# Kernel tuning notes

Measured on AMD Instinct MI355X. Metric: run time of the kernel, lower is better.

The kernel has to match this reference:

```python
import jax, jax.numpy as jnp
import numpy as np

B, T, S, C, E, H = 4, 2048, 2048, 256, 512, 8
D = E // H
SCALE = E ** (-0.5)


def setup_inputs() -> dict:
    key = jax.random.key(0)
    ks = jax.random.split(key, 12)
    x = jax.random.normal(ks[0], (B, T, C), dtype=jnp.float32)
    context = jax.random.normal(ks[1], (B, S, E), dtype=jnp.float32)
    pad_mask = jax.random.randint(ks[2], (B, T, S), 0, 2) == 1
    p = 0.02
    # Conv1d kernel_size=1 weights stored squeezed: [out_ch, in_ch]
    w_in = jax.random.normal(ks[3], (E, C), dtype=jnp.float32) * p
    b_in = jnp.zeros((E,), dtype=jnp.float32)
    wq = jax.random.normal(ks[4], (E, E), dtype=jnp.float32) * p
    bq = jnp.zeros((E,), dtype=jnp.float32)
    wk = jax.random.normal(ks[5], (E, E), dtype=jnp.float32) * p
    bk = jnp.zeros((E,), dtype=jnp.float32)
    wv = jax.random.normal(ks[6], (E, E), dtype=jnp.float32) * p
    bv = jnp.zeros((E,), dtype=jnp.float32)
    w_out = jax.random.normal(ks[7], (C, E), dtype=jnp.float32) * p
    b_out = jnp.zeros((C,), dtype=jnp.float32)
    return {"x": x, "context": context, "pad_mask": pad_mask,
            "w_in": w_in, "b_in": b_in, "wq": wq, "bq": bq,
            "wk": wk, "bk": bk, "wv": wv, "bv": bv,
            "w_out": w_out, "b_out": b_out}


def reference(x, context, pad_mask, w_in, b_in, wq, bq, wk, bk, wv, bv, w_out, b_out):
    # proj_in: Conv1d k=1 == per-token linear on channel dim. [B,T,C] -> [B,T,E]
    xe = jnp.einsum('btc,ec->bte', x, w_in) + b_in
    Q = (xe @ wq.T + bq).reshape(B, T, H, D)       # query tokens
    K = (context @ wk.T + bk).reshape(B, S, H, D)  # key tokens
    V = (context @ wv.T + bv).reshape(B, S, H, D)
    att = jnp.einsum('bihd,bjhd->bhij', Q, K) * SCALE  # [B,H,T,S]
    att = jnp.where(pad_mask[:, None, :, :], jnp.float32(-1e9), att)
    att = jax.nn.softmax(att, axis=-1)
    out = jnp.einsum('bhij,bjhd->bihd', att, V).reshape(B, T, E)
    # proj_out: Conv1d k=1, [B,T,E] -> [B,T,C]
    out = jnp.einsum('bte,ce->btc', out, w_out) + b_out
    return out
```

## Files before the change

### kernel.cpp

```cpp
#include <hip/hip_runtime.h>
#include <cstdint>
#include <cstddef>

#define Bb 4
#define Tt 2048
#define Ssz 2048
#define Cc 256
#define Ee 512
#define Hh 8
#define LDK 1024

typedef short bf8 __attribute__((ext_vector_type(8)));
typedef float f4 __attribute__((ext_vector_type(4)));

__device__ __forceinline__ unsigned short f2bf(float x) {
  unsigned int u = __float_as_uint(x);
  u += 0x7fffu + ((u >> 16) & 1u);
  return (unsigned short)(u >> 16);
}

template <bool OUT_BF16, int BM, int BN, int WGM>
__device__ __forceinline__ void gemm_core(unsigned short (*As)[72],
                                          unsigned short (*Bs)[72],
                                          const unsigned short* __restrict__ A,
                                          const unsigned short* __restrict__ Bt,
                                          const float* __restrict__ bias0,
                                          const float* __restrict__ bias1, int split,
                                          void* __restrict__ Cout,
                                          int M, int N, int K, int m0, int n0) {
  constexpr int WGN = 4 / WGM;
  constexpr int MI = BM / (WGM * 16);
  constexpr int NJ = BN / (WGN * 16);
  constexpr int NA = BM / 32;
  constexpr int NB = BN / 32;
  const int tid = threadIdx.x;
  const int wave = tid >> 6, lane = tid & 63;
  const int lrow = lane & 15, quad = lane >> 4;
  const int wm = (wave / WGN) * (BM / WGM);
  const int wn = (wave % WGN) * (BN / WGN);
  const int arow = tid >> 3, ac = tid & 7;

  f4 acc[MI][NJ];
#pragma unroll
  for (int i = 0; i < MI; i++)
#pragma unroll
    for (int j = 0; j < NJ; j++) {
      f4 z = {0.f, 0.f, 0.f, 0.f};
      acc[i][j] = z;
    }

  bf8 apre[NA], bpre[NB];
#pragma unroll
  for (int i = 0; i < NA; i++)
    apre[i] = *(const bf8*)(A + (size_t)(m0 + arow + i * 32) * K + ac * 8);
#pragma unroll
  for (int i = 0; i < NB; i++)
    bpre[i] = *(const bf8*)(Bt + (size_t)(n0 + arow + i * 32) * K + ac * 8);

  const int nkt = K >> 6;
  for (int kt = 0; kt < nkt; ++kt) {
#pragma unroll
    for (int i = 0; i < NA; i++) *(bf8*)&As[arow + i * 32][ac * 8] = apre[i];
#pragma unroll
    for (int i = 0; i < NB; i++) *(bf8*)&Bs[arow + i * 32][ac * 8] = bpre[i];
    __syncthreads();
    if (kt + 1 < nkt) {
      int k0 = (kt + 1) << 6;
#pragma unroll
      for (int i = 0; i < NA; i++)
        apre[i] = *(const bf8*)(A + (size_t)(m0 + arow + i * 32) * K + k0 + ac * 8);
#pragma unroll
      for (int i = 0; i < NB; i++)
        bpre[i] = *(const bf8*)(Bt + (size_t)(n0 + arow + i * 32) * K + k0 + ac * 8);
    }
#pragma unroll
    for (int kk = 0; kk < 2; kk++) {
      bf8 af[MI], bff[NJ];
#pragma unroll
      for (int i = 0; i < MI; i++)
        af[i] = *(const bf8*)&As[wm + i * 16 + lrow][kk * 32 + quad * 8];
#pragma unroll
      for (int j = 0; j < NJ; j++)
        bff[j] = *(const bf8*)&Bs[wn + j * 16 + lrow][kk * 32 + quad * 8];
#pragma unroll
      for (int i = 0; i < MI; i++)
#pragma unroll
        for (int j = 0; j < NJ; j++)
          acc[i][j] = __builtin_amdgcn_mfma_f32_16x16x32_bf16(af[i], bff[j],
                                                              acc[i][j], 0, 0, 0);
    }
    __syncthreads();
  }

#pragma unroll
  for (int j = 0; j < NJ; j++) {
    int col = n0 + wn + j * 16 + lrow;
    float bvv = 0.f;
    if (bias0) bvv = (col < split) ? bias0[col] : bias1[col - split];
#pragma unroll
    for (int i = 0; i < MI; i++) {
#pragma unroll
      for (int r = 0; r < 4; r++) {
        int row = m0 + wm + i * 16 + quad * 4 + r;
        float v = acc[i][j][r] + bvv;
        if (OUT_BF16)
          ((unsigned short*)Cout)[(size_t)row * N + col] = f2bf(v);
        else
          ((float*)Cout)[(size_t)row * N + col] = v;
      }
    }
  }
}

template <bool OUT_BF16, int BM, int BN, int WGM>
__global__ __launch_bounds__(256) void gemm_bt(const unsigned short* __restrict__ A,
                                               const unsigned short* __restrict__ Bt,
                                               const float* __restrict__ bias0,
                                               const float* __restrict__ bias1, int split,
                                               void* __restrict__ Cout,
                                               int M, int N, int K) {
  __shared__ unsigned short As[BM][72];
  __shared__ unsigned short Bs[BN][72];
  gemm_core<OUT_BF16, BM, BN, WGM>(As, Bs, A, Bt, bias0, bias1, split, Cout, M, N, K,
                                   blockIdx.x * BM, blockIdx.y * BN);
}

__global__ __launch_bounds__(256) void prep(const float* __restrict__ x,
                                            const float* __restrict__ ctx,
                                            const float* __restrict__ w_in,
                                            const float* __restrict__ b_in,
                                            const float* __restrict__ wq,
                                            const float* __restrict__ bq,
                                            const float* __restrict__ wk,
                                            const float* __restrict__ wv,
                                            const float* __restrict__ wo,
                                            unsigned short* __restrict__ xb,
                                            unsigned short* __restrict__ cb,
                                            unsigned short* __restrict__ wkvb,
                                            unsigned short* __restrict__ wob,
                                            unsigned short* __restrict__ wqin,
                                            float* __restrict__ bqinb, float qsc) {
  __shared__ unsigned short sh[128][72];
  const int bid = blockIdx.x, tid = threadIdx.x;
  if (bid < 6144) {
    const float* s;
    unsigned short* d;
    int i;
    if (bid < 2048) { s = x; d = xb; i = bid * 256 + tid; }
    else            { s = ctx; d = cb; i = (bid - 2048) * 256 + tid; }
    float4 v = ((const float4*)s)[i];
    ushort4 o;
    o.x = f2bf(v.x); o.y = f2bf(v.y); o.z = f2bf(v.z); o.w = f2bf(v.w);
    ((ushort4*)d)[i] = o;
  } else if (bid < 6784) {
    int i = (bid - 6144) * 256 + tid;
    const float* s;
    unsigned short* d;
    int off;
    if (i < 131072)      { s = wk; d = wkvb; off = i; }
    else                 { s = wo; d = wob; off = i - 131072; }
    if (i >= 65536 && i < 131072) { s = wv; off = i - 65536; d = wkvb + 262144; }
    float4 v = ((const float4*)s)[off];
    ushort4 o;
    o.x = f2bf(v.x); o.y = f2bf(v.y); o.z = f2bf(v.z); o.w = f2bf(v.w);
    ((ushort4*)d)[off] = o;
  } else if (bid < 6816) {
    const int idx = bid - 6784;
    const int m0 = (idx & 7) * 64, n0 = (idx >> 3) * 64;
    unsigned short (*As)[72] = (unsigned short (*)[72]) & sh[0][0];
    unsigned short (*Bs)[72] = (unsigned short (*)[72]) & sh[64][0];
    const int wave = tid >> 6, lane = tid & 63;
    const int lrow = lane & 15, quad = lane >> 4;
    const int wm = (wave >> 1) * 32, wn = (wave & 1) * 32;
    const int arow = tid >> 3, ac = tid & 7;
    f4 acc[2][2];
#pragma unroll
    for (int i = 0; i < 2; i++)
#pragma unroll
      for (int j = 0; j < 2; j++) {
        f4 z = {0.f, 0.f, 0.f, 0.f};
        acc[i][j] = z;
      }
    for (int kt = 0; kt < 8; kt++) {
#pragma unroll
      for (int i = 0; i < 2; i++) {
        int row = arow + i * 32;
        const float* src = wq + (size_t)(m0 + row) * Ee + kt * 64 + ac * 8;
        float4 v0 = *(const float4*)src, v1 = *(const float4*)(src + 4);
        bf8 av;
        av[0] = (short)f2bf(v0.x * qsc); av[1] = (short)f2bf(v0.y * qsc);
        av[2] = (short)f2bf(v0.z * qsc); av[3] = (short)f2bf(v0.w * qsc);
        av[4] = (short)f2bf(v1.x * qsc); av[5] = (short)f2bf(v1.y * qsc);
        av[6] = (short)f2bf(v1.z * qsc); av[7] = (short)f2bf(v1.w * qsc);
        *(bf8*)&As[row][ac * 8] = av;
        int c = n0 + row;
        bf8 bv;
#pragma unroll
        for (int k = 0; k < 8; k++)
          bv[k] = (short)f2bf(w_in[(size_t)(kt * 64 + ac * 8 + k) * Cc + c]);
        *(bf8*)&Bs[row][ac * 8] = bv;
      }
      __syncthreads();
#pragma unroll
      for (int kk = 0; kk < 2; kk++) {
        bf8 af[2], bff[2];
#pragma unroll
        for (int i = 0; i < 2; i++) af[i] = *(const bf8*)&As[wm + i * 16 + lrow][kk * 32 + quad * 8];
#pragma unroll
        for (int j = 0; j < 2; j++) bff[j] = *(const bf8*)&Bs[wn + j * 16 + lrow][kk * 32 + quad * 8];
#pragma unroll
        for (int i = 0; i < 2; i++)
#pragma unroll
          for (int j = 0; j < 2; j++)
            acc[i][j] = __builtin_amdgcn_mfma_f32_16x16x32_bf16(af[i], bff[j], acc[i][j], 0, 0, 0);
      }
      __syncthreads();
    }
#pragma unroll
    for (int j = 0; j < 2; j++)
#pragma unroll
      for (int i = 0; i < 2; i++)
#pragma unroll
        for (int r = 0; r < 4; r++)
          wqin[(size_t)(m0 + wm + i * 16 + quad * 4 + r) * Cc + n0 + wn + j * 16 + lrow] =
              f2bf(acc[i][j][r]);
  } else {
    const int o = (bid - 6816) * 32 + (tid >> 3);
    const int k0 = (tid & 7) * 64;
    float s = 0.f;
#pragma unroll
    for (int i = 0; i < 16; i++) {
      float4 w = *(const float4*)(wq + (size_t)o * Ee + k0 + i * 4);
      float4 bb = *(const float4*)(b_in + k0 + i * 4);
      s += w.x * bb.x + w.y * bb.y + w.z * bb.z + w.w * bb.w;
    }
    s += __shfl_xor(s, 1);
    s += __shfl_xor(s, 2);
    s += __shfl_xor(s, 4);
    if ((tid & 7) == 0) bqinb[o] = (s + bq[o]) * qsc;
  }
}

__global__ __launch_bounds__(256) void kvpack(const unsigned short* __restrict__ cb,
                                              const unsigned short* __restrict__ wkv,
                                              const float* __restrict__ bk,
                                              const float* __restrict__ bv,
                                              unsigned short* __restrict__ KVout,
                                              const int* __restrict__ mask,
                                              unsigned int* __restrict__ mp) {
  __shared__ unsigned short As[128][72];
  __shared__ unsigned short Bs[128][72];
  const int bid = blockIdx.x;
  if (bid < 512) {
    gemm_core<true, 128, 128, 2>(As, Bs, cb, wkv, bk, bv, 512, KVout, 8192, 1024, 512,
                                 (bid & 63) * 128, (bid >> 6) * 128);
  } else {
    int i = (bid - 512) * 256 + threadIdx.x;
    const int4* src = (const int4*)mask + (size_t)i * 8;
    unsigned int w = 0;
#pragma unroll
    for (int k = 0; k < 8; k++) {
      int4 v = src[k];
      w |= (unsigned int)(v.x != 0) << (k * 4);
      w |= (unsigned int)(v.y != 0) << (k * 4 + 1);
      w |= (unsigned int)(v.z != 0) << (k * 4 + 2);
      w |= (unsigned int)(v.w != 0) << (k * 4 + 3);
    }
    mp[i] = w;
  }
}

__global__ __launch_bounds__(256) void vtrans(const unsigned short* __restrict__ V, int ldv,
                                              unsigned short* __restrict__ Vt) {
  __shared__ unsigned short tile[64][72];
  const int tid = threadIdx.x;
  const int b = blockIdx.z, h = blockIdx.y, s0 = blockIdx.x * 64;
#pragma unroll
  for (int i = 0; i < 2; i++) {
    int id = tid + i * 256;
    int row = id >> 3, c = id & 7;
    *(bf8*)&tile[row][c * 8] =
        *(const bf8*)(V + (size_t)(b * Ssz + s0 + row) * ldv + h * 64 + c * 8);
  }
  __syncthreads();
#pragma unroll
  for (int i = 0; i < 2; i++) {
    int id = tid + i * 256;
    int d = id >> 3, c = id & 7;
    bf8 o;
#pragma unroll
    for (int k = 0; k < 8; k++) {
      int kk = (k + d) & 7;
      o[kk] = (short)tile[c * 8 + kk][d];
    }
    *(bf8*)(Vt + (size_t)((b * Hh + h) * 64 + d) * Ssz + s0 + c * 8) = o;
  }
}

__global__ __launch_bounds__(256) void attn(const unsigned short* __restrict__ Q,
                                            const unsigned short* __restrict__ K,
                                            const unsigned short* __restrict__ Vt,
                                            const unsigned int* __restrict__ mp,
                                            unsigned short* __restrict__ O) {
  __shared__ unsigned short Ks[2][64][72];
  __shared__ unsigned short Vts[2][64][72];
  __shared__ unsigned short Ps[128][72];
  const int tid = threadIdx.x;
  const int wave = tid >> 6, lane = tid & 63;
  const int lrow = lane & 15, quad = lane >> 4;
  const int b = blockIdx.z, h = blockIdx.y, t0 = blockIdx.x * 128;
  const int arow = tid >> 3, ac = tid & 7;
  const int wm = wave * 32;

#pragma unroll
  for (int i = 0; i < 4; i++) {
    int row = arow + i * 32;
    *(bf8*)&Ps[row][ac * 8] =
        *(const bf8*)(Q + (size_t)(b * Tt + t0 + row) * Ee + h * 64 + ac * 8);
  }
  __syncthreads();
  bf8 qf[2][2];
#pragma unroll
  for (int mi = 0; mi < 2; mi++) {
    qf[mi][0] = *(const bf8*)&Ps[wm + mi * 16 + lrow][quad * 8];
    qf[mi][1] = *(const bf8*)&Ps[wm + mi * 16 + lrow][32 + quad * 8];
  }

  f4 oacc[2][4];
  f4 dacc[2];
#pragma unroll
  for (int mi = 0; mi < 2; mi++) {
    f4 z = {0.f, 0.f, 0.f, 0.f};
    dacc[mi] = z;
#pragma unroll
    for (int j = 0; j < 4; j++) oacc[mi][j] = z;
  }
  bf8 ones;
#pragma unroll
  for (int k = 0; k < 8; k++) ones[k] = (short)0x3F80;

  const unsigned short* Kbase = K + (size_t)b * Ssz * LDK + h * 64;
  const unsigned short* Vbase = Vt + (size_t)((b * Hh + h) * 64) * Ssz;
  const unsigned int* mrow0 = mp + (size_t)(b * Tt + t0 + wm + lrow) * 64;
  const unsigned int* mrow1 = mp + (size_t)(b * Tt + t0 + wm + 16 + lrow) * 64;

  bf8 kreg[2], vreg[2];
#pragma unroll
  for (int i = 0; i < 2; i++) {
    int row = arow + i * 32;
    kreg[i] = *(const bf8*)(Kbase + (size_t)row * LDK + ac * 8);
    vreg[i] = *(const bf8*)(Vbase + (size_t)row * Ssz + ac * 8);
  }

  int buf = 0;
  for (int s0 = 0; s0 < Ssz; s0 += 64) {
#pragma unroll
    for (int i = 0; i < 2; i++) {
      int row = arow + i * 32;
      *(bf8*)&Ks[buf][row][ac * 8] = kreg[i];
      *(bf8*)&Vts[buf][row][ac * 8] = vreg[i];
    }
    __syncthreads();
    if (s0 + 64 < Ssz) {
#pragma unroll
      for (int i = 0; i < 2; i++) {
        int row = arow + i * 32;
        kreg[i] = *(const bf8*)(Kbase + (size_t)(s0 + 64 + row) * LDK + ac * 8);
        vreg[i] = *(const bf8*)(Vbase + (size_t)row * Ssz + s0 + 64 + ac * 8);
      }
    }
    const uint2 mw0 = *(const uint2*)(mrow0 + (s0 >> 5));
    const uint2 mw1 = *(const uint2*)(mrow1 + (s0 >> 5));

#pragma unroll
    for (int sf = 0; sf < 4; sf++) {
      bf8 kf0 = *(const bf8*)&Ks[buf][sf * 16 + lrow][quad * 8];
      bf8 kf1 = *(const bf8*)&Ks[buf][sf * 16 + lrow][32 + quad * 8];
      f4 sa[2];
      f4 z = {0.f, 0.f, 0.f, 0.f};
      sa[0] = z; sa[1] = z;
      sa[0] = __builtin_amdgcn_mfma_f32_16x16x32_bf16(kf0, qf[0][0], sa[0], 0, 0, 0);
      sa[0] = __builtin_amdgcn_mfma_f32_16x16x32_bf16(kf1, qf[0][1], sa[0], 0, 0, 0);
      sa[1] = __builtin_amdgcn_mfma_f32_16x16x32_bf16(kf0, qf[1][0], sa[1], 0, 0, 0);
      sa[1] = __builtin_amdgcn_mfma_f32_16x16x32_bf16(kf1, qf[1][1], sa[1], 0, 0, 0);
#pragma unroll
      for (int mi = 0; mi < 2; mi++) {
        const uint2 mw = mi ? mw1 : mw0;
        const unsigned int w = (sf >= 2) ? mw.y : mw.x;
        ushort4 pk;
#pragma unroll
        for (int r = 0; r < 4; r++) {
          const unsigned int bit = (sf & 1) * 16 + quad * 4 + r;
          float e = __builtin_amdgcn_exp2f(sa[mi][r]);
          float p = ((w >> bit) & 1u) ? 0.f : e;
          unsigned short pb = (unsigned short)(__float_as_uint(p) >> 16);
          if (r == 0) pk.x = pb;
          else if (r == 1) pk.y = pb;
          else if (r == 2) pk.z = pb;
          else pk.w = pb;
        }
        *(ushort4*)&Ps[wm + mi * 16 + lrow][sf * 16 + quad * 4] = pk;
      }
    }
#pragma unroll
    for (int kk = 0; kk < 2; kk++) {
      bf8 pf[2];
#pragma unroll
      for (int mi = 0; mi < 2; mi++) {
        pf[mi] = *(const bf8*)&Ps[wm + mi * 16 + lrow][kk * 32 + quad * 8];
        dacc[mi] = __builtin_amdgcn_mfma_f32_16x16x32_bf16(pf[mi], ones, dacc[mi], 0, 0, 0);
      }
#pragma unroll
      for (int j = 0; j < 4; j++) {
        bf8 vf = *(const bf8*)&Vts[buf][j * 16 + lrow][kk * 32 + quad * 8];
#pragma unroll
        for (int mi = 0; mi < 2; mi++)
          oacc[mi][j] = __builtin_amdgcn_mfma_f32_16x16x32_bf16(pf[mi], vf, oacc[mi][j], 0, 0, 0);
      }
    }
    buf ^= 1;
  }

#pragma unroll
  for (int mi = 0; mi < 2; mi++) {
#pragma unroll
    for (int r = 0; r < 4; r++) {
      float inv = 1.0f / dacc[mi][r];
      int row = b * Tt + t0 + wm + mi * 16 + quad * 4 + r;
#pragma unroll
      for (int j = 0; j < 4; j++)
        O[(size_t)row * Ee + h * 64 + j * 16 + lrow] = f2bf(oacc[mi][j][r] * inv);
    }
  }
}

extern "C" void kernel_launch(void* const* d_in, const int* in_sizes, int n_in,
                              void* d_out, int out_size, void* d_ws, size_t ws_size,
                              hipStream_t stream) {
  const float* x    = (const float*)d_in[0];
  const float* ctx  = (const float*)d_in[1];
  const int*   mask = (const int*)d_in[2];
  const float* w_in = (const float*)d_in[3];
  const float* b_in = (const float*)d_in[4];
  const float* wq   = (const float*)d_in[5];
  const float* bq   = (const float*)d_in[6];
  const float* wk   = (const float*)d_in[7];
  const float* bk   = (const float*)d_in[8];
  const float* wv   = (const float*)d_in[9];
  const float* bv   = (const float*)d_in[10];
  const float* wo   = (const float*)d_in[11];
  const float* bo   = (const float*)d_in[12];

  const float qsc = 0.04419417382415922f * 1.4426950408889634f;

  unsigned short* ws = (unsigned short*)d_ws;
  unsigned short* xb    = ws;
  unsigned short* cb    = ws + 2097152;
  unsigned short* wkvb  = ws + 6291456;
  unsigned short* wob   = ws + 6815744;
  unsigned short* wqin  = ws + 6946816;
  float*          bqinb = (float*)(ws + 7077888);
  unsigned short* Qb    = ws + 7208960;
  unsigned short* KVb   = ws + 11403264;
  unsigned short* Ob    = ws + 19791872;
  unsigned int*   maskp = (unsigned int*)xb;
  unsigned short* Vtb   = cb;

  prep<<<6832, 256, 0, stream>>>(x, ctx, w_in, b_in, wq, bq, wk, wv, wo,
                                 xb, cb, wkvb, wob, wqin, bqinb, qsc);
  gemm_bt<true, 128, 64, 2><<<dim3(64, 8), 256, 0, stream>>>(
      xb, wqin, bqinb, nullptr, 512, Qb, 8192, 512, 256);
  kvpack<<<2560, 256, 0, stream>>>(cb, wkvb, bk, bv, KVb, mask, maskp);
  vtrans<<<dim3(32, 8, 4), 256, 0, stream>>>(KVb + 512, LDK, Vtb);
  attn<<<dim3(16, 8, 4), 256, 0, stream>>>(Qb, KVb, Vtb, maskp, Ob);
  gemm_bt<false, 64, 64, 2><<<dim3(128, 4), 256, 0, stream>>>(
      Ob, wob, bo, nullptr, 256, d_out, 8192, 256, 512);
}
```

Measured before the change: 252.6 us.

## Fuse Q/K/V projections into one kernel with inline fp32 conversion and V-transpose epilogue

Removes the separate fp32-to-bf16 conversion pass for x and context by converting inside the GEMM A-tile load. Merges the Q and K/V projection GEMMs into one launch, and writes V directly in transposed layout so the vtrans kernel is dropped. Mask packing moves into prep. The attention kernel now handles 256 query rows per block (64 per wave), doubling register accumulators. This halves the grid, which may lower occupancy.

```diff
diff --git a/kernel.cpp b/kernel.cpp
--- a/kernel.cpp
+++ b/kernel.cpp
@@ -8,7 +8,6 @@
 #define Cc 256
 #define Ee 512
 #define Hh 8
-#define LDK 1024
 
 typedef short bf8 __attribute__((ext_vector_type(8)));
 typedef float f4 __attribute__((ext_vector_type(4)));
@@ -19,114 +18,16 @@
   return (unsigned short)(u >> 16);
 }
 
-template <bool OUT_BF16, int BM, int BN, int WGM>
-__device__ __forceinline__ void gemm_core(unsigned short (*As)[72],
-                                          unsigned short (*Bs)[72],
-                                          const unsigned short* __restrict__ A,
-                                          const unsigned short* __restrict__ Bt,
-                                          const float* __restrict__ bias0,
-                                          const float* __restrict__ bias1, int split,
-                                          void* __restrict__ Cout,
-                                          int M, int N, int K, int m0, int n0) {
-  constexpr int WGN = 4 / WGM;
-  constexpr int MI = BM / (WGM * 16);
-  constexpr int NJ = BN / (WGN * 16);
-  constexpr int NA = BM / 32;
-  constexpr int NB = BN / 32;
-  const int tid = threadIdx.x;
-  const int wave = tid >> 6, lane = tid & 63;
-  const int lrow = lane & 15, quad = lane >> 4;
-  const int wm = (wave / WGN) * (BM / WGM);
-  const int wn = (wave % WGN) * (BN / WGN);
-  const int arow = tid >> 3, ac = tid & 7;
-
-  f4 acc[MI][NJ];
-#pragma unroll
-  for (int i = 0; i < MI; i++)
-#pragma unroll
-    for (int j = 0; j < NJ; j++) {
-      f4 z = {0.f, 0.f, 0.f, 0.f};
-      acc[i][j] = z;
-    }
-
-  bf8 apre[NA], bpre[NB];
-#pragma unroll
-  for (int i = 0; i < NA; i++)
-    apre[i] = *(const bf8*)(A + (size_t)(m0 + arow + i * 32) * K + ac * 8);
-#pragma unroll
-  for (int i = 0; i < NB; i++)
-    bpre[i] = *(const bf8*)(Bt + (size_t)(n0 + arow + i * 32) * K + ac * 8);
-
-  const int nkt = K >> 6;
-  for (int kt = 0; kt < nkt; ++kt) {
-#pragma unroll
-    for (int i = 0; i < NA; i++) *(bf8*)&As[arow + i * 32][ac * 8] = apre[i];
-#pragma unroll
-    for (int i = 0; i < NB; i++) *(bf8*)&Bs[arow + i * 32][ac * 8] = bpre[i];
-    __syncthreads();
-    if (kt + 1 < nkt) {
-      int k0 = (kt + 1) << 6;
-#pragma unroll
-      for (int i = 0; i < NA; i++)
-        apre[i] = *(const bf8*)(A + (size_t)(m0 + arow + i * 32) * K + k0 + ac * 8);
-#pragma unroll
-      for (int i = 0; i < NB; i++)
-        bpre[i] = *(const bf8*)(Bt + (size_t)(n0 + arow + i * 32) * K + k0 + ac * 8);
-    }
-#pragma unroll
-    for (int kk = 0; kk < 2; kk++) {
-      bf8 af[MI], bff[NJ];
-#pragma unroll
-      for (int i = 0; i < MI; i++)
-        af[i] = *(const bf8*)&As[wm + i * 16 + lrow][kk * 32 + quad * 8];
-#pragma unroll
-      for (int j = 0; j < NJ; j++)
-        bff[j] = *(const bf8*)&Bs[wn + j * 16 + lrow][kk * 32 + quad * 8];
-#pragma unroll
-      for (int i = 0; i < MI; i++)
-#pragma unroll
-        for (int j = 0; j < NJ; j++)
-          acc[i][j] = __builtin_amdgcn_mfma_f32_16x16x32_bf16(af[i], bff[j],
-                                                              acc[i][j], 0, 0, 0);
-    }
-    __syncthreads();
-  }
-
-#pragma unroll
-  for (int j = 0; j < NJ; j++) {
-    int col = n0 + wn + j * 16 + lrow;
-    float bvv = 0.f;
-    if (bias0) bvv = (col < split) ? bias0[col] : bias1[col - split];
-#pragma unroll
-    for (int i = 0; i < MI; i++) {
-#pragma unroll
-      for (int r = 0; r < 4; r++) {
-        int row = m0 + wm + i * 16 + quad * 4 + r;
-        float v = acc[i][j][r] + bvv;
-        if (OUT_BF16)
-          ((unsigned short*)Cout)[(size_t)row * N + col] = f2bf(v);
-        else
-          ((float*)Cout)[(size_t)row * N + col] = v;
-      }
-    }
-  }
-}
-
-template <bool OUT_BF16, int BM, int BN, int WGM>
-__global__ __launch_bounds__(256) void gemm_bt(const unsigned short* __restrict__ A,
-                                               const unsigned short* __restrict__ Bt,
-                                               const float* __restrict__ bias0,
-                                               const float* __restrict__ bias1, int split,
-                                               void* __restrict__ Cout,
-                                               int M, int N, int K) {
-  __shared__ unsigned short As[BM][72];
-  __shared__ unsigned short Bs[BN][72];
-  gemm_core<OUT_BF16, BM, BN, WGM>(As, Bs, A, Bt, bias0, bias1, split, Cout, M, N, K,
-                                   blockIdx.x * BM, blockIdx.y * BN);
-}
-
-__global__ __launch_bounds__(256) void prep(const float* __restrict__ x,
-                                            const float* __restrict__ ctx,
+__device__ __forceinline__ bf8 cvt8(float4 a, float4 b) {
+  bf8 r;
+  r[0] = (short)f2bf(a.x); r[1] = (short)f2bf(a.y);
+  r[2] = (short)f2bf(a.z); r[3] = (short)f2bf(a.w);
+  r[4] = (short)f2bf(b.x); r[5] = (short)f2bf(b.y);
+  r[6] = (short)f2bf(b.z); r[7] = (short)f2bf(b.w);
+  return r;
+}
+
+__global__ __launch_bounds__(256) void prep(const int* __restrict__ mask,
                                             const float* __restrict__ w_in,
                                             const float* __restrict__ b_in,
                                             const float* __restrict__ wq,
@@ -134,38 +35,42 @@
                                             const float* __restrict__ wk,
                                             const float* __restrict__ wv,
                                             const float* __restrict__ wo,
-                                            unsigned short* __restrict__ xb,
-                                            unsigned short* __restrict__ cb,
+                                            unsigned int* __restrict__ mp,
                                             unsigned short* __restrict__ wkvb,
                                             unsigned short* __restrict__ wob,
                                             unsigned short* __restrict__ wqin,
                                             float* __restrict__ bqinb, float qsc) {
   __shared__ unsigned short sh[128][72];
   const int bid = blockIdx.x, tid = threadIdx.x;
-  if (bid < 6144) {
-    const float* s;
-    unsigned short* d;
-    int i;
-    if (bid < 2048) { s = x; d = xb; i = bid * 256 + tid; }
-    else            { s = ctx; d = cb; i = (bid - 2048) * 256 + tid; }
-    float4 v = ((const float4*)s)[i];
-    ushort4 o;
-    o.x = f2bf(v.x); o.y = f2bf(v.y); o.z = f2bf(v.z); o.w = f2bf(v.w);
-    ((ushort4*)d)[i] = o;
-  } else if (bid < 6784) {
-    int i = (bid - 6144) * 256 + tid;
-    const float* s;
-    unsigned short* d;
-    int off;
-    if (i < 131072)      { s = wk; d = wkvb; off = i; }
-    else                 { s = wo; d = wob; off = i - 131072; }
-    if (i >= 65536 && i < 131072) { s = wv; off = i - 65536; d = wkvb + 262144; }
+  if (bid < 2048) {
+    int i = bid * 256 + tid;
+    const int4* src = (const int4*)mask + (size_t)i * 8;
+    unsigned int w = 0;
+#pragma unroll
+    for (int k = 0; k < 8; k++) {
+      int4 v = src[k];
+      w |= (unsigned int)(v.x != 0) << (k * 4);
+      w |= (unsigned int)(v.y != 0) << (k * 4 + 1);
+      w |= (unsigned int)(v.z != 0) << (k * 4 + 2);
+      w |= (unsigned int)(v.w != 0) << (k * 4 + 3);
+    }
+    mp[i] = w;
+  } else if (bid < 2560) {
+    int i = (bid - 2048) * 256 + tid;
+    const float* s = (i < 65536) ? wk : wv;
+    int off = (i < 65536) ? i : i - 65536;
     float4 v = ((const float4*)s)[off];
     ushort4 o;
     o.x = f2bf(v.x); o.y = f2bf(v.y); o.z = f2bf(v.z); o.w = f2bf(v.w);
-    ((ushort4*)d)[off] = o;
-  } else if (bid < 6816) {
-    const int idx = bid - 6784;
+    ((ushort4*)wkvb)[i] = o;
+  } else if (bid < 2688) {
+    int i = (bid - 2560) * 256 + tid;
+    float4 v = ((const float4*)wo)[i];
+    ushort4 o;
+    o.x = f2bf(v.x); o.y = f2bf(v.y); o.z = f2bf(v.z); o.w = f2bf(v.w);
+    ((ushort4*)wob)[i] = o;
+  } else if (bid < 2720) {
+    const int idx = bid - 2688;
     const int m0 = (idx & 7) * 64, n0 = (idx >> 3) * 64;
     unsigned short (*As)[72] = (unsigned short (*)[72]) & sh[0][0];
     unsigned short (*Bs)[72] = (unsigned short (*)[72]) & sh[64][0];
@@ -225,7 +130,7 @@
           wqin[(size_t)(m0 + wm + i * 16 + quad * 4 + r) * Cc + n0 + wn + j * 16 + lrow] =
               f2bf(acc[i][j][r]);
   } else {
-    const int o = (bid - 6816) * 32 + (tid >> 3);
+    const int o = (bid - 2720) * 32 + (tid >> 3);
     const int k0 = (tid & 7) * 64;
     float s = 0.f;
 #pragma unroll
@@ -241,59 +146,222 @@
   }
 }
 
-__global__ __launch_bounds__(256) void kvpack(const unsigned short* __restrict__ cb,
-                                              const unsigned short* __restrict__ wkv,
-                                              const float* __restrict__ bk,
-                                              const float* __restrict__ bv,
-                                              unsigned short* __restrict__ KVout,
-                                              const int* __restrict__ mask,
-                                              unsigned int* __restrict__ mp) {
+__global__ __launch_bounds__(256) void qkv(const float* __restrict__ x,
+                                           const float* __restrict__ ctx,
+                                           const unsigned short* __restrict__ wqin,
+                                           const float* __restrict__ bqinb,
+                                           const unsigned short* __restrict__ wkv,
+                                           const float* __restrict__ bk,
+                                           const float* __restrict__ bv,
+                                           unsigned short* __restrict__ Qb,
+                                           unsigned short* __restrict__ Kb,
+                                           unsigned short* __restrict__ Vt) {
   __shared__ unsigned short As[128][72];
   __shared__ unsigned short Bs[128][72];
-  const int bid = blockIdx.x;
-  if (bid < 512) {
-    gemm_core<true, 128, 128, 2>(As, Bs, cb, wkv, bk, bv, 512, KVout, 8192, 1024, 512,
-                                 (bid & 63) * 128, (bid >> 6) * 128);
+  const int bid = blockIdx.x, tid = threadIdx.x;
+  const bool isQ = bid < 256;
+  const int idx = isQ ? bid : bid - 256;
+  const int m0 = (idx & 63) * 128;
+  const int n0 = (idx >> 6) * 128;
+  const int K = isQ ? 256 : 512;
+  const float* A = isQ ? x : ctx;
+  const unsigned short* Bt = isQ ? wqin : wkv;
+
+  const int wave = tid >> 6, lane = tid & 63;
+  const int lrow = lane & 15, quad = lane >> 4;
+  const int wm = (wave >> 1) * 64, wn = (wave & 1) * 64;
+  const int arow = tid >> 3, ac = tid & 7;
+
+  f4 acc[4][4];
+#pragma unroll
+  for (int i = 0; i < 4; i++)
+#pragma unroll
+    for (int j = 0; j < 4; j++) {
+      f4 z = {0.f, 0.f, 0.f, 0.f};
+      acc[i][j] = z;
+    }
+
+  float4 ap0[4], ap1[4];
+  bf8 bpre[4];
+#pragma unroll
+  for (int i = 0; i < 4; i++) {
+    const float* src = A + (size_t)(m0 + arow + i * 32) * K + ac * 8;
+    ap0[i] = *(const float4*)src;
+    ap1[i] = *(const float4*)(src + 4);
+    bpre[i] = *(const bf8*)(Bt + (size_t)(n0 + arow + i * 32) * K + ac * 8);
+  }
+
+  const int nkt = K >> 6;
+  for (int kt = 0; kt < nkt; ++kt) {
+#pragma unroll
+    for (int i = 0; i < 4; i++) {
+      *(bf8*)&As[arow + i * 32][ac * 8] = cvt8(ap0[i], ap1[i]);
+      *(bf8*)&Bs[arow + i * 32][ac * 8] = bpre[i];
+    }
+    __syncthreads();
+    if (kt + 1 < nkt) {
+      int k0 = (kt + 1) << 6;
+#pragma unroll
+      for (int i = 0; i < 4; i++) {
+        const float* src = A + (size_t)(m0 + arow + i * 32) * K + k0 + ac * 8;
+        ap0[i] = *(const float4*)src;
+        ap1[i] = *(const float4*)(src + 4);
+        bpre[i] = *(const bf8*)(Bt + (size_t)(n0 + arow + i * 32) * K + k0 + ac * 8);
+      }
+    }
+#pragma unroll
+    for (int kk = 0; kk < 2; kk++) {
+      bf8 af[4], bff[4];
+#pragma unroll
+      for (int i = 0; i < 4; i++)
+        af[i] = *(const bf8*)&As[wm + i * 16 + lrow][kk * 32 + quad * 8];
+#pragma unroll
+      for (int j = 0; j < 4; j++)
+        bff[j] = *(const bf8*)&Bs[wn + j * 16 + lrow][kk * 32 + quad * 8];
+#pragma unroll
+      for (int i = 0; i < 4; i++)
+#pragma unroll
+        for (int j = 0; j < 4; j++)
+          acc[i][j] = __builtin_amdgcn_mfma_f32_16x16x32_bf16(af[i], bff[j],
+                                                              acc[i][j], 0, 0, 0);
+    }
+    __syncthreads();
+  }
+
+  if (isQ) {
+#pragma unroll
+    for (int j = 0; j < 4; j++) {
+      int col = n0 + wn + j * 16 + lrow;
+      float bvv = bqinb[col];
+#pragma unroll
+      for (int i = 0; i < 4; i++)
+#pragma unroll
+        for (int r = 0; r < 4; r++)
+          Qb[(size_t)(m0 + wm + i * 16 + quad * 4 + r) * Ee + col] =
+              f2bf(acc[i][j][r] + bvv);
+    }
+  } else if (n0 < 512) {
+#pragma unroll
+    for (int j = 0; j < 4; j++) {
+      int col = n0 + wn + j * 16 + lrow;
+      float bvv = bk[col];
+#pragma unroll
+      for (int i = 0; i < 4; i++)
+#pragma unroll
+        for (int r = 0; r < 4; r++)
+          Kb[(size_t)(m0 + wm + i * 16 + quad * 4 + r) * Ee + col] =
+              f2bf(acc[i][j][r] + bvv);
+    }
   } else {
-    int i = (bid - 512) * 256 + threadIdx.x;
-    const int4* src = (const int4*)mask + (size_t)i * 8;
-    unsigned int w = 0;
-#pragma unroll
-    for (int k = 0; k < 8; k++) {
-      int4 v = src[k];
-      w |= (unsigned int)(v.x != 0) << (k * 4);
-      w |= (unsigned int)(v.y != 0) << (k * 4 + 1);
-      w |= (unsigned int)(v.z != 0) << (k * 4 + 2);
-      w |= (unsigned int)(v.w != 0) << (k * 4 + 3);
-    }
-    mp[i] = w;
-  }
-}
-
-__global__ __launch_bounds__(256) void vtrans(const unsigned short* __restrict__ V, int ldv,
-                                              unsigned short* __restrict__ Vt) {
-  __shared__ unsigned short tile[64][72];
+#pragma unroll
+    for (int j = 0; j < 4; j++) {
+      int d = n0 - 512 + wn + j * 16 + lrow;
+      int h = d >> 6, dd = d & 63;
+      float bvv = bv[d];
+#pragma unroll
+      for (int i = 0; i < 4; i++) {
+        int tok = m0 + wm + i * 16 + quad * 4;
+        int b = tok >> 11, sl = tok & 2047;
+        ushort4 pk;
+        pk.x = f2bf(acc[i][j][0] + bvv);
+        pk.y = f2bf(acc[i][j][1] + bvv);
+        pk.z = f2bf(acc[i][j][2] + bvv);
+        pk.w = f2bf(acc[i][j][3] + bvv);
+        *(ushort4*)(Vt + (size_t)((b * Hh + h) * 64 + dd) * Ssz + sl) = pk;
+      }
+    }
+  }
+}
+
+template <bool OUT_BF16, int BM, int BN, int WGM>
+__global__ __launch_bounds__(256) void gemm_bt(const unsigned short* __restrict__ A,
+                                               const unsigned short* __restrict__ Bt,
+                                               const float* __restrict__ bias0,
+                                               void* __restrict__ Cout,
+                                               int M, int N, int K) {
+  constexpr int WGN = 4 / WGM;
+  constexpr int MI = BM / (WGM * 16);
+  constexpr int NJ = BN / (WGN * 16);
+  constexpr int NA = BM / 32;
+  constexpr int NB = BN / 32;
+  __shared__ unsigned short As[BM][72];
+  __shared__ unsigned short Bs[BN][72];
   const int tid = threadIdx.x;
-  const int b = blockIdx.z, h = blockIdx.y, s0 = blockIdx.x * 64;
-#pragma unroll
-  for (int i = 0; i < 2; i++) {
-    int id = tid + i * 256;
-    int row = id >> 3, c = id & 7;
-    *(bf8*)&tile[row][c * 8] =
-        *(const bf8*)(V + (size_t)(b * Ssz + s0 + row) * ldv + h * 64 + c * 8);
-  }
-  __syncthreads();
-#pragma unroll
-  for (int i = 0; i < 2; i++) {
-    int id = tid + i * 256;
-    int d = id >> 3, c = id & 7;
-    bf8 o;
-#pragma unroll
-    for (int k = 0; k < 8; k++) {
-      int kk = (k + d) & 7;
-      o[kk] = (short)tile[c * 8 + kk][d];
-    }
-    *(bf8*)(Vt + (size_t)((b * Hh + h) * 64 + d) * Ssz + s0 + c * 8) = o;
+  const int wave = tid >> 6, lane = tid & 63;
+  const int lrow = lane & 15, quad = lane >> 4;
+  const int wm = (wave / WGN) * (BM / WGM);
+  const int wn = (wave % WGN) * (BN / WGN);
+  const int m0 = blockIdx.x * BM, n0 = blockIdx.y * BN;
+  const int arow = tid >> 3, ac = tid & 7;
+
+  f4 acc[MI][NJ];
+#pragma unroll
+  for (int i = 0; i < MI; i++)
+#pragma unroll
+    for (int j = 0; j < NJ; j++) {
+      f4 z = {0.f, 0.f, 0.f, 0.f};
+      acc[i][j] = z;
+    }
+
+  bf8 apre[NA], bpre[NB];
+#pragma unroll
+  for (int i = 0; i < NA; i++)
+    apre[i] = *(const bf8*)(A + (size_t)(m0 + arow + i * 32) * K + ac * 8);
+#pragma unroll
+  for (int i = 0; i < NB; i++)
+    bpre[i] = *(const bf8*)(Bt + (size_t)(n0 + arow + i * 32) * K + ac * 8);
+
+  const int nkt = K >> 6;
+  for (int kt = 0; kt < nkt; ++kt) {
+#pragma unroll
+    for (int i = 0; i < NA; i++) *(bf8*)&As[arow + i * 32][ac * 8] = apre[i];
+#pragma unroll
+    for (int i = 0; i < NB; i++) *(bf8*)&Bs[arow + i * 32][ac * 8] = bpre[i];
+    __syncthreads();
+    if (kt + 1 < nkt) {
+      int k0 = (kt + 1) << 6;
+#pragma unroll
+      for (int i = 0; i < NA; i++)
+        apre[i] = *(const bf8*)(A + (size_t)(m0 + arow + i * 32) * K + k0 + ac * 8);
+#pragma unroll
+      for (int i = 0; i < NB; i++)
+        bpre[i] = *(const bf8*)(Bt + (size_t)(n0 + arow + i * 32) * K + k0 + ac * 8);
+    }
+#pragma unroll
+    for (int kk = 0; kk < 2; kk++) {
+      bf8 af[MI], bff[NJ];
+#pragma unroll
+      for (int i = 0; i < MI; i++)
+        af[i] = *(const bf8*)&As[wm + i * 16 + lrow][kk * 32 + quad * 8];
+#pragma unroll
+      for (int j = 0; j < NJ; j++)
+        bff[j] = *(const bf8*)&Bs[wn + j * 16 + lrow][kk * 32 + quad * 8];
+#pragma unroll
+      for (int i = 0; i < MI; i++)
+#pragma unroll
+        for (int j = 0; j < NJ; j++)
+          acc[i][j] = __builtin_amdgcn_mfma_f32_16x16x32_bf16(af[i], bff[j],
+                                                              acc[i][j], 0, 0, 0);
+    }
+    __syncthreads();
+  }
+
+#pragma unroll
+  for (int j = 0; j < NJ; j++) {
+    int col = n0 + wn + j * 16 + lrow;
+    float bvv = bias0 ? bias0[col] : 0.f;
+#pragma unroll
+    for (int i = 0; i < MI; i++) {
+#pragma unroll
+      for (int r = 0; r < 4; r++) {
+        int row = m0 + wm + i * 16 + quad * 4 + r;
+        float v = acc[i][j][r] + bvv;
+        if (OUT_BF16)
+          ((unsigned short*)Cout)[(size_t)row * N + col] = f2bf(v);
+        else
+          ((float*)Cout)[(size_t)row * N + col] = v;
+      }
+    }
   }
 }
 
@@ -304,32 +372,32 @@
                                             unsigned short* __restrict__ O) {
   __shared__ unsigned short Ks[2][64][72];
   __shared__ unsigned short Vts[2][64][72];
-  __shared__ unsigned short Ps[128][72];
+  __shared__ unsigned short Ps[256][72];
   const int tid = threadIdx.x;
   const int wave = tid >> 6, lane = tid & 63;
   const int lrow = lane & 15, quad = lane >> 4;
-  const int b = blockIdx.z, h = blockIdx.y, t0 = blockIdx.x * 128;
+  const int b = blockIdx.z, h = blockIdx.y, t0 = blockIdx.x * 256;
   const int arow = tid >> 3, ac = tid & 7;
-  const int wm = wave * 32;
-
-#pragma unroll
-  for (int i = 0; i < 4; i++) {
+  const int wm = wave * 64;
+
+#pragma unroll
+  for (int i = 0; i < 8; i++) {
     int row = arow + i * 32;
     *(bf8*)&Ps[row][ac * 8] =
         *(const bf8*)(Q + (size_t)(b * Tt + t0 + row) * Ee + h * 64 + ac * 8);
   }
   __syncthreads();
-  bf8 qf[2][2];
-#pragma unroll
-  for (int mi = 0; mi < 2; mi++) {
+  bf8 qf[4][2];
+#pragma unroll
+  for (int mi = 0; mi < 4; mi++) {
     qf[mi][0] = *(const bf8*)&Ps[wm + mi * 16 + lrow][quad * 8];
     qf[mi][1] = *(const bf8*)&Ps[wm + mi * 16 + lrow][32 + quad * 8];
   }
 
-  f4 oacc[2][4];
-  f4 dacc[2];
-#pragma unroll
-  for (int mi = 0; mi < 2; mi++) {
+  f4 oacc[4][4];
+  f4 dacc[4];
+#pragma unroll
+  for (int mi = 0; mi < 4; mi++) {
     f4 z = {0.f, 0.f, 0.f, 0.f};
     dacc[mi] = z;
 #pragma unroll
@@ -339,16 +407,18 @@
 #pragma unroll
   for (int k = 0; k < 8; k++) ones[k] = (short)0x3F80;
 
-  const unsigned short* Kbase = K + (size_t)b * Ssz * LDK + h * 64;
+  const unsigned short* Kbase = K + (size_t)b * Ssz * Ee + h * 64;
   const unsigned short* Vbase = Vt + (size_t)((b * Hh + h) * 64) * Ssz;
-  const unsigned int* mrow0 = mp + (size_t)(b * Tt + t0 + wm + lrow) * 64;
-  const unsigned int* mrow1 = mp + (size_t)(b * Tt + t0 + wm + 16 + lrow) * 64;
+  const unsigned int* mrow[4];
+#pragma unroll
+  for (int mi = 0; mi < 4; mi++)
+    mrow[mi] = mp + (size_t)(b * Tt + t0 + wm + mi * 16 + lrow) * 64;
 
   bf8 kreg[2], vreg[2];
 #pragma unroll
   for (int i = 0; i < 2; i++) {
     int row = arow + i * 32;
-    kreg[i] = *(const bf8*)(Kbase + (size_t)row * LDK + ac * 8);
+    kreg[i] = *(const bf8*)(Kbase + (size_t)row * Ee + ac * 8);
     vreg[i] = *(const bf8*)(Vbase + (size_t)row * Ssz + ac * 8);
   }
 
@@ -365,28 +435,29 @@
 #pragma unroll
       for (int i = 0; i < 2; i++) {
         int row = arow + i * 32;
-        kreg[i] = *(const bf8*)(Kbase + (size_t)(s0 + 64 + row) * LDK + ac * 8);
+        kreg[i] = *(const bf8*)(Kbase + (size_t)(s0 + 64 + row) * Ee + ac * 8);
         vreg[i] = *(const bf8*)(Vbase + (size_t)row * Ssz + s0 + 64 + ac * 8);
       }
     }
-    const uint2 mw0 = *(const uint2*)(mrow0 + (s0 >> 5));
-    const uint2 mw1 = *(const uint2*)(mrow1 + (s0 >> 5));
+    uint2 mw[4];
+#pragma unroll
+    for (int mi = 0; mi < 4; mi++) mw[mi] = *(const uint2*)(mrow[mi] + (s0 >> 5));
 
 #pragma unroll
     for (int sf = 0; sf < 4; sf++) {
       bf8 kf0 = *(const bf8*)&Ks[buf][sf * 16 + lrow][quad * 8];
       bf8 kf1 = *(const bf8*)&Ks[buf][sf * 16 + lrow][32 + quad * 8];
-      f4 sa[2];
-      f4 z = {0.f, 0.f, 0.f, 0.f};
-      sa[0] = z; sa[1] = z;
-      sa[0] = __builtin_amdgcn_mfma_f32_16x16x32_bf16(kf0, qf[0][0], sa[0], 0, 0, 0);
-      sa[0] = __builtin_amdgcn_mfma_f32_16x16x32_bf16(kf1, qf[0][1], sa[0], 0, 0, 0);
-      sa[1] = __builtin_amdgcn_mfma_f32_16x16x32_bf16(kf0, qf[1][0], sa[1], 0, 0, 0);
-      sa[1] = __builtin_amdgcn_mfma_f32_16x16x32_bf16(kf1, qf[1][1], sa[1], 0, 0, 0);
-#pragma unroll
-      for (int mi = 0; mi < 2; mi++) {
-        const uint2 mw = mi ? mw1 : mw0;
-        const unsigned int w = (sf >= 2) ? mw.y : mw.x;
+      f4 sa[4];
+#pragma unroll
+      for (int mi = 0; mi < 4; mi++) {
+        f4 z = {0.f, 0.f, 0.f, 0.f};
+        sa[mi] = z;
+        sa[mi] = __builtin_amdgcn_mfma_f32_16x16x32_bf16(kf0, qf[mi][0], sa[mi], 0, 0, 0);
+        sa[mi] = __builtin_amdgcn_mfma_f32_16x16x32_bf16(kf1, qf[mi][1], sa[mi], 0, 0, 0);
+      }
+#pragma unroll
+      for (int mi = 0; mi < 4; mi++) {
+        const unsigned int w = (sf >= 2) ? mw[mi].y : mw[mi].x;
         ushort4 pk;
 #pragma unroll
         for (int r = 0; r < 4; r++) {
@@ -404,9 +475,9 @@
     }
 #pragma unroll
     for (int kk = 0; kk < 2; kk++) {
-      bf8 pf[2];
-#pragma unroll
-      for (int mi = 0; mi < 2; mi++) {
+      bf8 pf[4];
+#pragma unroll
+      for (int mi = 0; mi < 4; mi++) {
         pf[mi] = *(const bf8*)&Ps[wm + mi * 16 + lrow][kk * 32 + quad * 8];
         dacc[mi] = __builtin_amdgcn_mfma_f32_16x16x32_bf16(pf[mi], ones, dacc[mi], 0, 0, 0);
       }
@@ -414,7 +485,7 @@
       for (int j = 0; j < 4; j++) {
         bf8 vf = *(const bf8*)&Vts[buf][j * 16 + lrow][kk * 32 + quad * 8];
 #pragma unroll
-        for (int mi = 0; mi < 2; mi++)
+        for (int mi = 0; mi < 4; mi++)
           oacc[mi][j] = __builtin_amdgcn_mfma_f32_16x16x32_bf16(pf[mi], vf, oacc[mi][j], 0, 0, 0);
       }
     }
@@ -422,7 +493,7 @@
   }
 
 #pragma unroll
-  for (int mi = 0; mi < 2; mi++) {
+  for (int mi = 0; mi < 4; mi++) {
 #pragma unroll
     for (int r = 0; r < 4; r++) {
       float inv = 1.0f / dacc[mi][r];
@@ -454,25 +525,20 @@
   const float qsc = 0.04419417382415922f * 1.4426950408889634f;
 
   unsigned short* ws = (unsigned short*)d_ws;
-  unsigned short* xb    = ws;
-  unsigned short* cb    = ws + 2097152;
-  unsigned short* wkvb  = ws + 6291456;
-  unsigned short* wob   = ws + 6815744;
-  unsigned short* wqin  = ws + 6946816;
-  float*          bqinb = (float*)(ws + 7077888);
-  unsigned short* Qb    = ws + 7208960;
-  unsigned short* KVb   = ws + 11403264;
-  unsigned short* Ob    = ws + 19791872;
-  unsigned int*   maskp = (unsigned int*)xb;
-  unsigned short* Vtb   = cb;
-
-  prep<<<6832, 256, 0, stream>>>(x, ctx, w_in, b_in, wq, bq, wk, wv, wo,
-                                 xb, cb, wkvb, wob, wqin, bqinb, qsc);
-  gemm_bt<true, 128, 64, 2><<<dim3(64, 8), 256, 0, stream>>>(
-      xb, wqin, bqinb, nullptr, 512, Qb, 8192, 512, 256);
-  kvpack<<<2560, 256, 0, stream>>>(cb, wkvb, bk, bv, KVb, mask, maskp);
-  vtrans<<<dim3(32, 8, 4), 256, 0, stream>>>(KVb + 512, LDK, Vtb);
-  attn<<<dim3(16, 8, 4), 256, 0, stream>>>(Qb, KVb, Vtb, maskp, Ob);
+  unsigned int*   maskp = (unsigned int*)ws;
+  unsigned short* wkvb  = ws + 1048576;
+  unsigned short* wob   = ws + 1572864;
+  unsigned short* wqin  = ws + 1703936;
+  float*          bqinb = (float*)(ws + 1835008);
+  unsigned short* Qb    = ws + 1836032;
+  unsigned short* Kb    = ws + 6030336;
+  unsigned short* Vtb   = ws + 10224640;
+  unsigned short* Ob    = ws + 14418944;
+
+  prep<<<2736, 256, 0, stream>>>(mask, w_in, b_in, wq, bq, wk, wv, wo,
+                                 maskp, wkvb, wob, wqin, bqinb, qsc);
+  qkv<<<768, 256, 0, stream>>>(x, ctx, wqin, bqinb, wkvb, bk, bv, Qb, Kb, Vtb);
+  attn<<<dim3(8, 8, 4), 256, 0, stream>>>(Qb, Kb, Vtb, maskp, Ob);
   gemm_bt<false, 64, 64, 2><<<dim3(128, 4), 256, 0, stream>>>(
-      Ob, wob, bo, nullptr, 256, d_out, 8192, 256, 512);
-}
+      Ob, wob, bo, d_out, 8192, 256, 512);
+}
```

Result: slower. 264.0 us (+4.5%).
